# Optimization experiments

Hardware: AMD Instinct MI355X
Metric: run time of the kernel (lower is better)

The kernel has to match this reference:

```python
import jax, jax.numpy as jnp
import numpy as np

WS = 8          # window size
NUM_HEADS = 8


def setup_inputs() -> dict:
    key = jax.random.key(0)
    k1, k2, k3 = jax.random.split(key, 3)
    B, H, W, C = 8, 192, 192, 256
    x = jax.random.normal(k1, (B, H, W, C), dtype=jnp.float32)
    w_qkv = jax.random.normal(k2, (3 * C, C), dtype=jnp.float32) * (C ** -0.5)
    b_qkv = jnp.zeros((3 * C,), dtype=jnp.float32)
    w_proj = jax.random.normal(k3, (C, C), dtype=jnp.float32) * (C ** -0.5)
    b_proj = jnp.zeros((C,), dtype=jnp.float32)
    return {"x": x, "w_qkv": w_qkv, "b_qkv": b_qkv, "w_proj": w_proj, "b_proj": b_proj}


def _mhsa(tokens, w_qkv, b_qkv, w_proj, b_proj):
    # tokens: [Bgrp, N, C]
    Bg, N, C = tokens.shape
    d = C // NUM_HEADS
    qkv = tokens @ w_qkv.T + b_qkv                      # [Bg, N, 3C]
    qkv = qkv.reshape(Bg, N, 3, NUM_HEADS, d)
    q, k, v = [jnp.transpose(qkv[:, :, i], (0, 2, 1, 3)) for i in range(3)]  # [Bg, h, N, d]
    attn = jax.nn.softmax(jnp.einsum('bhnd,bhmd->bhnm', q, k) * (d ** -0.5), axis=-1)
    out = jnp.einsum('bhnm,bhmd->bhnd', attn, v)        # [Bg, h, N, d]
    out = jnp.transpose(out, (0, 2, 1, 3)).reshape(Bg, N, C)
    return out @ w_proj.T + b_proj


def reference(x, w_qkv, b_qkv, w_proj, b_proj):
    B, H, W, C = x.shape
    nH, nW = H // WS, W // WS
    # window partition: [B, H, W, C] -> [B*nH*nW, WS, WS, C]
    g = x.reshape(B, nH, WS, nW, WS, C).transpose(0, 1, 3, 2, 4, 5)
    tokens = g.reshape(B * nH * nW, WS * WS, C)
    tokens = _mhsa(tokens, w_qkv, b_qkv, w_proj, b_proj)
    # window unpartition
    g = tokens.reshape(B, nH, nW, WS, WS, C).transpose(0, 1, 3, 2, 4, 5)
    return g.reshape(B, H, W, C)
```

## Files before the change

### kernel.cpp

```cpp
#include <hip/hip_runtime.h>

typedef _Float16 half8  __attribute__((ext_vector_type(8)));
typedef _Float16 half4_t __attribute__((ext_vector_type(4)));
typedef __fp16   fp16x2 __attribute__((ext_vector_type(2)));
typedef float    f32x4  __attribute__((ext_vector_type(4)));

union PKU  { fp16x2 h; int i; };
union PK2  { fp16x2 h[2]; int i[2]; half4_t h4; };

__device__ __forceinline__ half4_t mk4(int a, int b) {
  PK2 u; u.i[0] = a; u.i[1] = b; return u.h4;
}

__device__ __forceinline__ int tokIdx(int r, int c) { return r*256 + (c ^ ((r & 7) << 3)); }

__global__ void __launch_bounds__(256)
wconv_kernel(const float* __restrict__ wq, const float* __restrict__ wp,
             _Float16* __restrict__ o)
{
  const int i = blockIdx.x * 256 + threadIdx.x;
  if (i < 768*256) o[i] = (_Float16)wq[i];
  else             o[i] = (_Float16)wp[i - 768*256];
}

__global__ void __launch_bounds__(256, 2)
attn_kernel(const float* __restrict__ x,
            const float* __restrict__ b_qkv,
            const float* __restrict__ b_proj,
            const _Float16* __restrict__ w16,
            float* __restrict__ out)
{
  __shared__ __align__(16) _Float16 tok[64*256];

  const int tid  = threadIdx.x;
  const int lane = tid & 63;
  const int w    = tid >> 6;
  const int l15  = lane & 15;
  const int g    = lane >> 4;

  const int wid = blockIdx.x;
  const int b   = wid / (24*24);
  const int wh  = (wid / 24) % 24;
  const int ww  = wid % 24;
  const long long base = (((long long)b*192 + wh*8)*192 + ww*8)*256;

#pragma unroll
  for (int i = 0; i < 16; ++i) {
    const int tk = w*16 + i;
    const float4 v = *(const float4*)(x + base + ((tk >> 3)*192 + (tk & 7))*256 + lane*4);
    half4_t h;
    h[0] = (_Float16)v.x; h[1] = (_Float16)v.y;
    h[2] = (_Float16)v.z; h[3] = (_Float16)v.w;
    *(half4_t*)(tok + tk*256 + ((lane*4) ^ ((tk & 7) << 3))) = h;
  }
  __syncthreads();

  const _Float16* wqkv16  = w16;
  const _Float16* wproj16 = w16 + 768*256;

  int ohp[2][2][4][2];

#pragma unroll
  for (int hi = 0; hi < 2; ++hi) {
    const int hd = 2*w + hi;

    f32x4 qa[2][4], kc[2][4], vv[4][2];
#pragma unroll
    for (int mi = 0; mi < 2; ++mi)
#pragma unroll
      for (int ni = 0; ni < 4; ++ni) { qa[mi][ni] = (f32x4)0.0f; kc[mi][ni] = (f32x4)0.0f; }
#pragma unroll
    for (int mi = 0; mi < 4; ++mi)
#pragma unroll
      for (int ni = 0; ni < 2; ++ni) vv[mi][ni] = (f32x4)0.0f;

#pragma unroll
    for (int kk = 0; kk < 8; ++kk) {
      half8 bt[4], aw[4], wv[2];
#pragma unroll
      for (int ni = 0; ni < 4; ++ni)
        bt[ni] = *(const half8*)(tok + tokIdx(ni*16 + l15, kk*32 + g*8));
#pragma unroll
      for (int mi = 0; mi < 2; ++mi) {
        aw[mi]     = *(const half8*)(wqkv16 + (      hd*32 + mi*16 + l15)*256 + kk*32 + g*8);
        aw[2 + mi] = *(const half8*)(wqkv16 + (256 + hd*32 + mi*16 + l15)*256 + kk*32 + g*8);
        wv[mi]     = *(const half8*)(wqkv16 + (512 + hd*32 + mi*16 + l15)*256 + kk*32 + g*8);
      }
      __builtin_amdgcn_s_setprio(1);
#pragma unroll
      for (int mi = 0; mi < 2; ++mi)
#pragma unroll
        for (int ni = 0; ni < 4; ++ni) {
          qa[mi][ni] = __builtin_amdgcn_mfma_f32_16x16x32_f16(aw[mi],     bt[ni], qa[mi][ni], 0, 0, 0);
          kc[mi][ni] = __builtin_amdgcn_mfma_f32_16x16x32_f16(aw[2 + mi], bt[ni], kc[mi][ni], 0, 0, 0);
        }
#pragma unroll
      for (int mi = 0; mi < 4; ++mi)
#pragma unroll
        for (int ni = 0; ni < 2; ++ni)
          vv[mi][ni] = __builtin_amdgcn_mfma_f32_16x16x32_f16(bt[mi], wv[ni], vv[mi][ni], 0, 0, 0);
      __builtin_amdgcn_s_setprio(0);
    }

    int qtp[2][4][2];
#pragma unroll
    for (int mi = 0; mi < 2; ++mi) {
      float bq[4];
#pragma unroll
      for (int r = 0; r < 4; ++r) bq[r] = b_qkv[hd*32 + mi*16 + g*4 + r];
#pragma unroll
      for (int ni = 0; ni < 4; ++ni) {
        PKU u0, u1;
        u0.h = __builtin_amdgcn_cvt_pkrtz(qa[mi][ni][0] + bq[0], qa[mi][ni][1] + bq[1]);
        u1.h = __builtin_amdgcn_cvt_pkrtz(qa[mi][ni][2] + bq[2], qa[mi][ni][3] + bq[3]);
        qtp[mi][ni][0] = u0.i; qtp[mi][ni][1] = u1.i;
      }
    }

    int kcp[2][4][2];
#pragma unroll
    for (int mi = 0; mi < 2; ++mi) {
      float bk[4];
#pragma unroll
      for (int r = 0; r < 4; ++r) bk[r] = b_qkv[256 + hd*32 + mi*16 + g*4 + r];
#pragma unroll
      for (int ni = 0; ni < 4; ++ni) {
        PKU u0, u1;
        u0.h = __builtin_amdgcn_cvt_pkrtz(kc[mi][ni][0] + bk[0], kc[mi][ni][1] + bk[1]);
        u1.h = __builtin_amdgcn_cvt_pkrtz(kc[mi][ni][2] + bk[2], kc[mi][ni][3] + bk[3]);
        kcp[mi][ni][0] = u0.i; kcp[mi][ni][1] = u1.i;
      }
    }

    int vpk[4][2][2];
#pragma unroll
    for (int ni = 0; ni < 2; ++ni) {
      const float bv = b_qkv[512 + hd*32 + ni*16 + l15];
#pragma unroll
      for (int mi = 0; mi < 4; ++mi) {
        PKU u0, u1;
        u0.h = __builtin_amdgcn_cvt_pkrtz(vv[mi][ni][0] + bv, vv[mi][ni][1] + bv);
        u1.h = __builtin_amdgcn_cvt_pkrtz(vv[mi][ni][2] + bv, vv[mi][ni][3] + bv);
        vpk[mi][ni][0] = u0.i;
        vpk[mi][ni][1] = u1.i;
      }
    }

    int pk[4][4][2];
    float rv[4];
    {
      f32x4 s[4][4];
#pragma unroll
      for (int MI = 0; MI < 4; ++MI)
#pragma unroll
        for (int ni = 0; ni < 4; ++ni) s[MI][ni] = (f32x4)0.0f;
      __builtin_amdgcn_s_setprio(1);
#pragma unroll
      for (int kk2 = 0; kk2 < 2; ++kk2)
#pragma unroll
        for (int ni = 0; ni < 4; ++ni) {
          const half4_t qb = mk4(qtp[kk2][ni][0], qtp[kk2][ni][1]);
#pragma unroll
          for (int MI = 0; MI < 4; ++MI)
            s[MI][ni] = __builtin_amdgcn_mfma_f32_16x16x16f16(
                mk4(kcp[kk2][MI][0], kcp[kk2][MI][1]), qb, s[MI][ni], 0, 0, 0);
        }
      __builtin_amdgcn_s_setprio(0);

      const float alpha = 0.17677669529663687f;
#pragma unroll
      for (int ni = 0; ni < 4; ++ni) {
        float m = s[0][ni][0];
#pragma unroll
        for (int MI = 0; MI < 4; ++MI)
#pragma unroll
          for (int r = 0; r < 4; ++r) m = fmaxf(m, s[MI][ni][r]);
        m = fmaxf(m, __shfl_xor(m, 16, 64));
        m = fmaxf(m, __shfl_xor(m, 32, 64));
        float sum = 0.0f;
#pragma unroll
        for (int MI = 0; MI < 4; ++MI)
#pragma unroll
          for (int r = 0; r < 4; ++r) {
            const float e = __expf((s[MI][ni][r] - m) * alpha);
            sum += e;
            s[MI][ni][r] = e;
          }
        sum += __shfl_xor(sum, 16, 64);
        sum += __shfl_xor(sum, 32, 64);
        rv[ni] = 1.0f / sum;
#pragma unroll
        for (int MI = 0; MI < 4; ++MI) {
          PKU u0, u1;
          u0.h = __builtin_amdgcn_cvt_pkrtz(s[MI][ni][0], s[MI][ni][1]);
          u1.h = __builtin_amdgcn_cvt_pkrtz(s[MI][ni][2], s[MI][ni][3]);
          pk[MI][ni][0] = u0.i;
          pk[MI][ni][1] = u1.i;
        }
      }
    }

    {
      f32x4 oh[2][4];
#pragma unroll
      for (int MI = 0; MI < 2; ++MI)
#pragma unroll
        for (int ni = 0; ni < 4; ++ni) oh[MI][ni] = (f32x4)0.0f;
      __builtin_amdgcn_s_setprio(1);
#pragma unroll
      for (int kk2 = 0; kk2 < 4; ++kk2)
#pragma unroll
        for (int ni = 0; ni < 4; ++ni) {
          const half4_t pb = mk4(pk[kk2][ni][0], pk[kk2][ni][1]);
#pragma unroll
          for (int MI = 0; MI < 2; ++MI)
            oh[MI][ni] = __builtin_amdgcn_mfma_f32_16x16x16f16(
                mk4(vpk[kk2][MI][0], vpk[kk2][MI][1]), pb, oh[MI][ni], 0, 0, 0);
        }
      __builtin_amdgcn_s_setprio(0);
#pragma unroll
      for (int MI = 0; MI < 2; ++MI)
#pragma unroll
        for (int ni = 0; ni < 4; ++ni) {
          PK2 u;
          u.h[0] = __builtin_amdgcn_cvt_pkrtz(oh[MI][ni][0] * rv[ni], oh[MI][ni][1] * rv[ni]);
          u.h[1] = __builtin_amdgcn_cvt_pkrtz(oh[MI][ni][2] * rv[ni], oh[MI][ni][3] * rv[ni]);
          ohp[hi][MI][ni][0] = u.i[0];
          ohp[hi][MI][ni][1] = u.i[1];
        }
    }
  }

  __syncthreads();

#pragma unroll
  for (int hi = 0; hi < 2; ++hi) {
    const int hd = 2*w + hi;
#pragma unroll
    for (int MI = 0; MI < 2; ++MI)
#pragma unroll
      for (int ni = 0; ni < 4; ++ni) {
        PK2 u;
        u.i[0] = ohp[hi][MI][ni][0];
        u.i[1] = ohp[hi][MI][ni][1];
        *(half4_t*)(tok + tokIdx(ni*16 + l15, hd*32 + MI*16 + g*4)) = u.h4;
      }
  }
  __syncthreads();

  f32x4 pa[4][4];
#pragma unroll
  for (int mi = 0; mi < 4; ++mi)
#pragma unroll
    for (int ni = 0; ni < 4; ++ni) pa[mi][ni] = (f32x4)0.0f;

#pragma unroll
  for (int kk = 0; kk < 8; ++kk) {
    half8 af[4], bf[4];
#pragma unroll
    for (int mi = 0; mi < 4; ++mi)
      af[mi] = *(const half8*)(tok + tokIdx(mi*16 + l15, kk*32 + g*8));
#pragma unroll
    for (int ni = 0; ni < 4; ++ni)
      bf[ni] = *(const half8*)(wproj16 + (w*64 + ni*16 + l15)*256 + kk*32 + g*8);
    __builtin_amdgcn_s_setprio(1);
#pragma unroll
    for (int mi = 0; mi < 4; ++mi)
#pragma unroll
      for (int ni = 0; ni < 4; ++ni)
        pa[mi][ni] = __builtin_amdgcn_mfma_f32_16x16x32_f16(af[mi], bf[ni], pa[mi][ni], 0, 0, 0);
    __builtin_amdgcn_s_setprio(0);
  }

#pragma unroll
  for (int ni = 0; ni < 4; ++ni) {
    const float bb = b_proj[w*64 + ni*16 + l15];
#pragma unroll
    for (int mi = 0; mi < 4; ++mi)
#pragma unroll
      for (int r = 0; r < 4; ++r) pa[mi][ni][r] += bb;
  }

  float* tokF = (float*)tok;
#pragma unroll
  for (int p = 0; p < 2; ++p) {
    __syncthreads();
#pragma unroll
    for (int mh = 0; mh < 2; ++mh) {
      const int mi = 2*p + mh;
#pragma unroll
      for (int ni = 0; ni < 4; ++ni)
#pragma unroll
        for (int r = 0; r < 4; ++r) {
          const int tr = mh*16 + g*4 + r;
          tokF[tr*256 + ((w*64 + ni*16 + l15) ^ ((tr & 7) << 2))] = pa[mi][ni][r];
        }
    }
    __syncthreads();
#pragma unroll
    for (int i = 0; i < 8; ++i) {
      const int tr = w*8 + i;
      const int t  = p*32 + tr;
      const long long rowbase = base + ((long long)(t >> 3)*192 + (t & 7))*256;
      const f32x4 v4 = *(const f32x4*)(tokF + tr*256 + ((lane*4) ^ ((tr & 7) << 2)));
      *(f32x4*)(out + rowbase + lane*4) = v4;
    }
  }
}

extern "C" void kernel_launch(void* const* d_in, const int* in_sizes, int n_in,
                              void* d_out, int out_size, void* d_ws, size_t ws_size,
                              hipStream_t stream) {
  const float* x      = (const float*)d_in[0];
  const float* w_qkv  = (const float*)d_in[1];
  const float* b_qkv  = (const float*)d_in[2];
  const float* w_proj = (const float*)d_in[3];
  const float* b_proj = (const float*)d_in[4];
  float* out = (float*)d_out;
  _Float16* w16 = (_Float16*)d_ws;

  wconv_kernel<<<1024, 256, 0, stream>>>(w_qkv, w_proj, w16);
  attn_kernel<<<4608, 256, 0, stream>>>(x, b_qkv, b_proj, w16, out);
}
```

Measured before the change: 356.5 us.

## Process two windows per block and prefetch the second window's input during compute

Each block now handles two adjacent windows, using a double-buffered LDS tile. The second window's x loads are issued in stages, interleaved with the first window's attention compute, and converted into the second buffer before it is needed, so global-load latency is hidden behind MFMA work. The weight conversion kernel is also vectorised to write 8 halves per thread. In exchange, LDS per block doubles to 64KB, which may limit occupancy at two blocks per CU, the extra prefetch registers add register pressure, and the grid is halved.

```diff
diff --git a/kernel.cpp b/kernel.cpp
--- a/kernel.cpp
+++ b/kernel.cpp
@@ -18,10 +18,22 @@
 wconv_kernel(const float* __restrict__ wq, const float* __restrict__ wp,
              _Float16* __restrict__ o)
 {
-  const int i = blockIdx.x * 256 + threadIdx.x;
-  if (i < 768*256) o[i] = (_Float16)wq[i];
-  else             o[i] = (_Float16)wp[i - 768*256];
+  const int i = (blockIdx.x * 256 + threadIdx.x) * 8;
+  const float4 a = *(const float4*)((i < 768*256 ? wq + i : wp + (i - 768*256)));
+  const float4 b = *(const float4*)((i < 768*256 ? wq + i + 4 : wp + (i - 768*256) + 4));
+  half8 h;
+  h[0] = (_Float16)a.x; h[1] = (_Float16)a.y; h[2] = (_Float16)a.z; h[3] = (_Float16)a.w;
+  h[4] = (_Float16)b.x; h[5] = (_Float16)b.y; h[6] = (_Float16)b.z; h[7] = (_Float16)b.w;
+  *(half8*)(o + i) = h;
 }
+
+#define LDX(s, j) (*(const f32x4*)(x + base1 + (((w*16 + (s)*4 + (j)) >> 3)*192 + ((w*16 + (s)*4 + (j)) & 7))*256 + lane*4))
+#define PF_ISSUE(s) { pf[0] = LDX(s,0); pf[1] = LDX(s,1); pf[2] = LDX(s,2); pf[3] = LDX(s,3); }
+#define STH(s, j) { const int tk = w*16 + (s)*4 + (j); half4_t h; \
+  h[0] = (_Float16)pf[j][0]; h[1] = (_Float16)pf[j][1]; \
+  h[2] = (_Float16)pf[j][2]; h[3] = (_Float16)pf[j][3]; \
+  *(half4_t*)(tok1 + tk*256 + ((lane*4) ^ ((tk & 7) << 3))) = h; }
+#define PF_COMMIT(s) { STH(s,0) STH(s,1) STH(s,2) STH(s,3) }
 
 __global__ void __launch_bounds__(256, 2)
 attn_kernel(const float* __restrict__ x,
@@ -30,7 +42,7 @@
             const _Float16* __restrict__ w16,
             float* __restrict__ out)
 {
-  __shared__ __align__(16) _Float16 tok[64*256];
+  __shared__ __align__(16) _Float16 tokbuf[2][64*256];
 
   const int tid  = threadIdx.x;
   const int lane = tid & 63;
@@ -38,273 +50,295 @@
   const int l15  = lane & 15;
   const int g    = lane >> 4;
 
-  const int wid = blockIdx.x;
-  const int b   = wid / (24*24);
-  const int wh  = (wid / 24) % 24;
-  const int ww  = wid % 24;
-  const long long base = (((long long)b*192 + wh*8)*192 + ww*8)*256;
+  const int W0  = blockIdx.x * 2;
+  const int b   = W0 / (24*24);
+  const int wh  = (W0 / 24) % 24;
+  const int ww  = W0 % 24;
+  const long long base0 = (((long long)b*192 + wh*8)*192 + ww*8)*256;
+  const long long base1 = base0 + 2048;
+
+  const _Float16* wqkv16  = w16;
+  const _Float16* wproj16 = w16 + 768*256;
+  _Float16* tok1 = &tokbuf[1][0];
+
+  f32x4 pf[4];
 
 #pragma unroll
   for (int i = 0; i < 16; ++i) {
     const int tk = w*16 + i;
-    const float4 v = *(const float4*)(x + base + ((tk >> 3)*192 + (tk & 7))*256 + lane*4);
+    const f32x4 v = *(const f32x4*)(x + base0 + ((tk >> 3)*192 + (tk & 7))*256 + lane*4);
     half4_t h;
-    h[0] = (_Float16)v.x; h[1] = (_Float16)v.y;
-    h[2] = (_Float16)v.z; h[3] = (_Float16)v.w;
-    *(half4_t*)(tok + tk*256 + ((lane*4) ^ ((tk & 7) << 3))) = h;
+    h[0] = (_Float16)v[0]; h[1] = (_Float16)v[1];
+    h[2] = (_Float16)v[2]; h[3] = (_Float16)v[3];
+    *(half4_t*)(tokbuf[0] + tk*256 + ((lane*4) ^ ((tk & 7) << 3))) = h;
   }
   __syncthreads();
 
-  const _Float16* wqkv16  = w16;
-  const _Float16* wproj16 = w16 + 768*256;
-
-  int ohp[2][2][4][2];
-
-#pragma unroll
-  for (int hi = 0; hi < 2; ++hi) {
-    const int hd = 2*w + hi;
-
-    f32x4 qa[2][4], kc[2][4], vv[4][2];
-#pragma unroll
-    for (int mi = 0; mi < 2; ++mi)
-#pragma unroll
-      for (int ni = 0; ni < 4; ++ni) { qa[mi][ni] = (f32x4)0.0f; kc[mi][ni] = (f32x4)0.0f; }
-#pragma unroll
-    for (int mi = 0; mi < 4; ++mi)
-#pragma unroll
-      for (int ni = 0; ni < 2; ++ni) vv[mi][ni] = (f32x4)0.0f;
-
-#pragma unroll
-    for (int kk = 0; kk < 8; ++kk) {
-      half8 bt[4], aw[4], wv[2];
-#pragma unroll
-      for (int ni = 0; ni < 4; ++ni)
-        bt[ni] = *(const half8*)(tok + tokIdx(ni*16 + l15, kk*32 + g*8));
+#pragma unroll
+  for (int wi = 0; wi < 2; ++wi) {
+    _Float16* tokc = &tokbuf[wi][0];
+    const long long basec = (wi == 0) ? base0 : base1;
+
+    int ohp[2][2][4][2];
+
+#pragma unroll
+    for (int hi = 0; hi < 2; ++hi) {
+      const int hd = 2*w + hi;
+
+      f32x4 qa[2][4], kc[2][4], vv[4][2];
+#pragma unroll
+      for (int mi = 0; mi < 2; ++mi)
+#pragma unroll
+        for (int ni = 0; ni < 4; ++ni) { qa[mi][ni] = (f32x4)0.0f; kc[mi][ni] = (f32x4)0.0f; }
+#pragma unroll
+      for (int mi = 0; mi < 4; ++mi)
+#pragma unroll
+        for (int ni = 0; ni < 2; ++ni) vv[mi][ni] = (f32x4)0.0f;
+
+#pragma unroll
+      for (int kk = 0; kk < 8; ++kk) {
+        half8 bt[4], aw[4], wvr[2];
+#pragma unroll
+        for (int ni = 0; ni < 4; ++ni)
+          bt[ni] = *(const half8*)(tokc + tokIdx(ni*16 + l15, kk*32 + g*8));
+#pragma unroll
+        for (int mi = 0; mi < 2; ++mi) {
+          aw[mi]     = *(const half8*)(wqkv16 + (      hd*32 + mi*16 + l15)*256 + kk*32 + g*8);
+          aw[2 + mi] = *(const half8*)(wqkv16 + (256 + hd*32 + mi*16 + l15)*256 + kk*32 + g*8);
+          wvr[mi]    = *(const half8*)(wqkv16 + (512 + hd*32 + mi*16 + l15)*256 + kk*32 + g*8);
+        }
+        __builtin_amdgcn_s_setprio(1);
+#pragma unroll
+        for (int mi = 0; mi < 2; ++mi)
+#pragma unroll
+          for (int ni = 0; ni < 4; ++ni) {
+            qa[mi][ni] = __builtin_amdgcn_mfma_f32_16x16x32_f16(aw[mi],     bt[ni], qa[mi][ni], 0, 0, 0);
+            kc[mi][ni] = __builtin_amdgcn_mfma_f32_16x16x32_f16(aw[2 + mi], bt[ni], kc[mi][ni], 0, 0, 0);
+          }
+#pragma unroll
+        for (int mi = 0; mi < 4; ++mi)
+#pragma unroll
+          for (int ni = 0; ni < 2; ++ni)
+            vv[mi][ni] = __builtin_amdgcn_mfma_f32_16x16x32_f16(bt[mi], wvr[ni], vv[mi][ni], 0, 0, 0);
+        __builtin_amdgcn_s_setprio(0);
+      }
+
+      if (wi == 0) {
+        if (hi == 0) { PF_ISSUE(0) }
+        else         { PF_COMMIT(1) PF_ISSUE(2) }
+      }
+
+      int qtp[2][4][2];
 #pragma unroll
       for (int mi = 0; mi < 2; ++mi) {
-        aw[mi]     = *(const half8*)(wqkv16 + (      hd*32 + mi*16 + l15)*256 + kk*32 + g*8);
-        aw[2 + mi] = *(const half8*)(wqkv16 + (256 + hd*32 + mi*16 + l15)*256 + kk*32 + g*8);
-        wv[mi]     = *(const half8*)(wqkv16 + (512 + hd*32 + mi*16 + l15)*256 + kk*32 + g*8);
-      }
-      __builtin_amdgcn_s_setprio(1);
-#pragma unroll
-      for (int mi = 0; mi < 2; ++mi)
+        float bq[4];
+#pragma unroll
+        for (int r = 0; r < 4; ++r) bq[r] = b_qkv[hd*32 + mi*16 + g*4 + r];
 #pragma unroll
         for (int ni = 0; ni < 4; ++ni) {
-          qa[mi][ni] = __builtin_amdgcn_mfma_f32_16x16x32_f16(aw[mi],     bt[ni], qa[mi][ni], 0, 0, 0);
-          kc[mi][ni] = __builtin_amdgcn_mfma_f32_16x16x32_f16(aw[2 + mi], bt[ni], kc[mi][ni], 0, 0, 0);
-        }
-#pragma unroll
-      for (int mi = 0; mi < 4; ++mi)
-#pragma unroll
-        for (int ni = 0; ni < 2; ++ni)
-          vv[mi][ni] = __builtin_amdgcn_mfma_f32_16x16x32_f16(bt[mi], wv[ni], vv[mi][ni], 0, 0, 0);
-      __builtin_amdgcn_s_setprio(0);
-    }
-
-    int qtp[2][4][2];
-#pragma unroll
-    for (int mi = 0; mi < 2; ++mi) {
-      float bq[4];
-#pragma unroll
-      for (int r = 0; r < 4; ++r) bq[r] = b_qkv[hd*32 + mi*16 + g*4 + r];
-#pragma unroll
-      for (int ni = 0; ni < 4; ++ni) {
-        PKU u0, u1;
-        u0.h = __builtin_amdgcn_cvt_pkrtz(qa[mi][ni][0] + bq[0], qa[mi][ni][1] + bq[1]);
-        u1.h = __builtin_amdgcn_cvt_pkrtz(qa[mi][ni][2] + bq[2], qa[mi][ni][3] + bq[3]);
-        qtp[mi][ni][0] = u0.i; qtp[mi][ni][1] = u1.i;
-      }
-    }
-
-    int kcp[2][4][2];
-#pragma unroll
-    for (int mi = 0; mi < 2; ++mi) {
-      float bk[4];
-#pragma unroll
-      for (int r = 0; r < 4; ++r) bk[r] = b_qkv[256 + hd*32 + mi*16 + g*4 + r];
-#pragma unroll
-      for (int ni = 0; ni < 4; ++ni) {
-        PKU u0, u1;
-        u0.h = __builtin_amdgcn_cvt_pkrtz(kc[mi][ni][0] + bk[0], kc[mi][ni][1] + bk[1]);
-        u1.h = __builtin_amdgcn_cvt_pkrtz(kc[mi][ni][2] + bk[2], kc[mi][ni][3] + bk[3]);
-        kcp[mi][ni][0] = u0.i; kcp[mi][ni][1] = u1.i;
-      }
-    }
-
-    int vpk[4][2][2];
-#pragma unroll
-    for (int ni = 0; ni < 2; ++ni) {
-      const float bv = b_qkv[512 + hd*32 + ni*16 + l15];
-#pragma unroll
-      for (int mi = 0; mi < 4; ++mi) {
-        PKU u0, u1;
-        u0.h = __builtin_amdgcn_cvt_pkrtz(vv[mi][ni][0] + bv, vv[mi][ni][1] + bv);
-        u1.h = __builtin_amdgcn_cvt_pkrtz(vv[mi][ni][2] + bv, vv[mi][ni][3] + bv);
-        vpk[mi][ni][0] = u0.i;
-        vpk[mi][ni][1] = u1.i;
-      }
-    }
-
-    int pk[4][4][2];
-    float rv[4];
-    {
-      f32x4 s[4][4];
-#pragma unroll
-      for (int MI = 0; MI < 4; ++MI)
-#pragma unroll
-        for (int ni = 0; ni < 4; ++ni) s[MI][ni] = (f32x4)0.0f;
-      __builtin_amdgcn_s_setprio(1);
-#pragma unroll
-      for (int kk2 = 0; kk2 < 2; ++kk2)
+          PKU u0, u1;
+          u0.h = __builtin_amdgcn_cvt_pkrtz(qa[mi][ni][0] + bq[0], qa[mi][ni][1] + bq[1]);
+          u1.h = __builtin_amdgcn_cvt_pkrtz(qa[mi][ni][2] + bq[2], qa[mi][ni][3] + bq[3]);
+          qtp[mi][ni][0] = u0.i; qtp[mi][ni][1] = u1.i;
+        }
+      }
+
+      int kcp[2][4][2];
+#pragma unroll
+      for (int mi = 0; mi < 2; ++mi) {
+        float bk[4];
+#pragma unroll
+        for (int r = 0; r < 4; ++r) bk[r] = b_qkv[256 + hd*32 + mi*16 + g*4 + r];
 #pragma unroll
         for (int ni = 0; ni < 4; ++ni) {
-          const half4_t qb = mk4(qtp[kk2][ni][0], qtp[kk2][ni][1]);
+          PKU u0, u1;
+          u0.h = __builtin_amdgcn_cvt_pkrtz(kc[mi][ni][0] + bk[0], kc[mi][ni][1] + bk[1]);
+          u1.h = __builtin_amdgcn_cvt_pkrtz(kc[mi][ni][2] + bk[2], kc[mi][ni][3] + bk[3]);
+          kcp[mi][ni][0] = u0.i; kcp[mi][ni][1] = u1.i;
+        }
+      }
+
+      int vpk[4][2][2];
+#pragma unroll
+      for (int ni = 0; ni < 2; ++ni) {
+        const float bv = b_qkv[512 + hd*32 + ni*16 + l15];
+#pragma unroll
+        for (int mi = 0; mi < 4; ++mi) {
+          PKU u0, u1;
+          u0.h = __builtin_amdgcn_cvt_pkrtz(vv[mi][ni][0] + bv, vv[mi][ni][1] + bv);
+          u1.h = __builtin_amdgcn_cvt_pkrtz(vv[mi][ni][2] + bv, vv[mi][ni][3] + bv);
+          vpk[mi][ni][0] = u0.i;
+          vpk[mi][ni][1] = u1.i;
+        }
+      }
+
+      int pk[4][4][2];
+      float rv[4];
+      {
+        f32x4 s[4][4];
+#pragma unroll
+        for (int MI = 0; MI < 4; ++MI)
+#pragma unroll
+          for (int ni = 0; ni < 4; ++ni) s[MI][ni] = (f32x4)0.0f;
+        __builtin_amdgcn_s_setprio(1);
+#pragma unroll
+        for (int kk2 = 0; kk2 < 2; ++kk2)
+#pragma unroll
+          for (int ni = 0; ni < 4; ++ni) {
+            const half4_t qb = mk4(qtp[kk2][ni][0], qtp[kk2][ni][1]);
+#pragma unroll
+            for (int MI = 0; MI < 4; ++MI)
+              s[MI][ni] = __builtin_amdgcn_mfma_f32_16x16x16f16(
+                  mk4(kcp[kk2][MI][0], kcp[kk2][MI][1]), qb, s[MI][ni], 0, 0, 0);
+          }
+        __builtin_amdgcn_s_setprio(0);
+
+        const float alpha = 0.17677669529663687f;
+#pragma unroll
+        for (int ni = 0; ni < 4; ++ni) {
+          float m = s[0][ni][0];
 #pragma unroll
           for (int MI = 0; MI < 4; ++MI)
-            s[MI][ni] = __builtin_amdgcn_mfma_f32_16x16x16f16(
-                mk4(kcp[kk2][MI][0], kcp[kk2][MI][1]), qb, s[MI][ni], 0, 0, 0);
-        }
-      __builtin_amdgcn_s_setprio(0);
-
-      const float alpha = 0.17677669529663687f;
-#pragma unroll
-      for (int ni = 0; ni < 4; ++ni) {
-        float m = s[0][ni][0];
-#pragma unroll
-        for (int MI = 0; MI < 4; ++MI)
-#pragma unroll
-          for (int r = 0; r < 4; ++r) m = fmaxf(m, s[MI][ni][r]);
-        m = fmaxf(m, __shfl_xor(m, 16, 64));
-        m = fmaxf(m, __shfl_xor(m, 32, 64));
-        float sum = 0.0f;
-#pragma unroll
-        for (int MI = 0; MI < 4; ++MI)
-#pragma unroll
-          for (int r = 0; r < 4; ++r) {
-            const float e = __expf((s[MI][ni][r] - m) * alpha);
-            sum += e;
-            s[MI][ni][r] = e;
-          }
-        sum += __shfl_xor(sum, 16, 64);
-        sum += __shfl_xor(sum, 32, 64);
-        rv[ni] = 1.0f / sum;
-#pragma unroll
-        for (int MI = 0; MI < 4; ++MI) {
-          PKU u0, u1;
-          u0.h = __builtin_amdgcn_cvt_pkrtz(s[MI][ni][0], s[MI][ni][1]);
-          u1.h = __builtin_amdgcn_cvt_pkrtz(s[MI][ni][2], s[MI][ni][3]);
-          pk[MI][ni][0] = u0.i;
-          pk[MI][ni][1] = u1.i;
-        }
-      }
-    }
-
-    {
-      f32x4 oh[2][4];
-#pragma unroll
-      for (int MI = 0; MI < 2; ++MI)
-#pragma unroll
-        for (int ni = 0; ni < 4; ++ni) oh[MI][ni] = (f32x4)0.0f;
-      __builtin_amdgcn_s_setprio(1);
-#pragma unroll
-      for (int kk2 = 0; kk2 < 4; ++kk2)
-#pragma unroll
-        for (int ni = 0; ni < 4; ++ni) {
-          const half4_t pb = mk4(pk[kk2][ni][0], pk[kk2][ni][1]);
-#pragma unroll
-          for (int MI = 0; MI < 2; ++MI)
-            oh[MI][ni] = __builtin_amdgcn_mfma_f32_16x16x16f16(
-                mk4(vpk[kk2][MI][0], vpk[kk2][MI][1]), pb, oh[MI][ni], 0, 0, 0);
-        }
-      __builtin_amdgcn_s_setprio(0);
+#pragma unroll
+            for (int r = 0; r < 4; ++r) m = fmaxf(m, s[MI][ni][r]);
+          m = fmaxf(m, __shfl_xor(m, 16, 64));
+          m = fmaxf(m, __shfl_xor(m, 32, 64));
+          float sum = 0.0f;
+#pragma unroll
+          for (int MI = 0; MI < 4; ++MI)
+#pragma unroll
+            for (int r = 0; r < 4; ++r) {
+              const float e = __expf((s[MI][ni][r] - m) * alpha);
+              sum += e;
+              s[MI][ni][r] = e;
+            }
+          sum += __shfl_xor(sum, 16, 64);
+          sum += __shfl_xor(sum, 32, 64);
+          rv[ni] = 1.0f / sum;
+#pragma unroll
+          for (int MI = 0; MI < 4; ++MI) {
+            PKU u0, u1;
+            u0.h = __builtin_amdgcn_cvt_pkrtz(s[MI][ni][0], s[MI][ni][1]);
+            u1.h = __builtin_amdgcn_cvt_pkrtz(s[MI][ni][2], s[MI][ni][3]);
+            pk[MI][ni][0] = u0.i;
+            pk[MI][ni][1] = u1.i;
+          }
+        }
+      }
+
+      {
+        f32x4 oh[2][4];
+#pragma unroll
+        for (int MI = 0; MI < 2; ++MI)
+#pragma unroll
+          for (int ni = 0; ni < 4; ++ni) oh[MI][ni] = (f32x4)0.0f;
+        __builtin_amdgcn_s_setprio(1);
+#pragma unroll
+        for (int kk2 = 0; kk2 < 4; ++kk2)
+#pragma unroll
+          for (int ni = 0; ni < 4; ++ni) {
+            const half4_t pb = mk4(pk[kk2][ni][0], pk[kk2][ni][1]);
+#pragma unroll
+            for (int MI = 0; MI < 2; ++MI)
+              oh[MI][ni] = __builtin_amdgcn_mfma_f32_16x16x16f16(
+                  mk4(vpk[kk2][MI][0], vpk[kk2][MI][1]), pb, oh[MI][ni], 0, 0, 0);
+          }
+        __builtin_amdgcn_s_setprio(0);
+#pragma unroll
+        for (int MI = 0; MI < 2; ++MI)
+#pragma unroll
+          for (int ni = 0; ni < 4; ++ni) {
+            PK2 u;
+            u.h[0] = __builtin_amdgcn_cvt_pkrtz(oh[MI][ni][0] * rv[ni], oh[MI][ni][1] * rv[ni]);
+            u.h[1] = __builtin_amdgcn_cvt_pkrtz(oh[MI][ni][2] * rv[ni], oh[MI][ni][3] * rv[ni]);
+            ohp[hi][MI][ni][0] = u.i[0];
+            ohp[hi][MI][ni][1] = u.i[1];
+          }
+      }
+
+      if (wi == 0) {
+        if (hi == 0) { PF_COMMIT(0) PF_ISSUE(1) }
+        else         { PF_COMMIT(2) PF_ISSUE(3) }
+      }
+    }
+
+    __syncthreads();
+
+#pragma unroll
+    for (int hi = 0; hi < 2; ++hi) {
+      const int hd = 2*w + hi;
 #pragma unroll
       for (int MI = 0; MI < 2; ++MI)
 #pragma unroll
         for (int ni = 0; ni < 4; ++ni) {
           PK2 u;
-          u.h[0] = __builtin_amdgcn_cvt_pkrtz(oh[MI][ni][0] * rv[ni], oh[MI][ni][1] * rv[ni]);
-          u.h[1] = __builtin_amdgcn_cvt_pkrtz(oh[MI][ni][2] * rv[ni], oh[MI][ni][3] * rv[ni]);
-          ohp[hi][MI][ni][0] = u.i[0];
-          ohp[hi][MI][ni][1] = u.i[1];
-        }
-    }
-  }
-
-  __syncthreads();
-
-#pragma unroll
-  for (int hi = 0; hi < 2; ++hi) {
-    const int hd = 2*w + hi;
-#pragma unroll
-    for (int MI = 0; MI < 2; ++MI)
-#pragma unroll
-      for (int ni = 0; ni < 4; ++ni) {
-        PK2 u;
-        u.i[0] = ohp[hi][MI][ni][0];
-        u.i[1] = ohp[hi][MI][ni][1];
-        *(half4_t*)(tok + tokIdx(ni*16 + l15, hd*32 + MI*16 + g*4)) = u.h4;
-      }
-  }
-  __syncthreads();
-
-  f32x4 pa[4][4];
-#pragma unroll
-  for (int mi = 0; mi < 4; ++mi)
-#pragma unroll
-    for (int ni = 0; ni < 4; ++ni) pa[mi][ni] = (f32x4)0.0f;
-
-#pragma unroll
-  for (int kk = 0; kk < 8; ++kk) {
-    half8 af[4], bf[4];
+          u.i[0] = ohp[hi][MI][ni][0];
+          u.i[1] = ohp[hi][MI][ni][1];
+          *(half4_t*)(tokc + tokIdx(ni*16 + l15, hd*32 + MI*16 + g*4)) = u.h4;
+        }
+    }
+    if (wi == 0) { PF_COMMIT(3) }
+    __syncthreads();
+
+    f32x4 pa[4][4];
 #pragma unroll
     for (int mi = 0; mi < 4; ++mi)
-      af[mi] = *(const half8*)(tok + tokIdx(mi*16 + l15, kk*32 + g*8));
-#pragma unroll
-    for (int ni = 0; ni < 4; ++ni)
-      bf[ni] = *(const half8*)(wproj16 + (w*64 + ni*16 + l15)*256 + kk*32 + g*8);
-    __builtin_amdgcn_s_setprio(1);
-#pragma unroll
-    for (int mi = 0; mi < 4; ++mi)
+#pragma unroll
+      for (int ni = 0; ni < 4; ++ni) pa[mi][ni] = (f32x4)0.0f;
+
+#pragma unroll
+    for (int kk = 0; kk < 8; ++kk) {
+      half8 af[4], bf[4];
+#pragma unroll
+      for (int mi = 0; mi < 4; ++mi)
+        af[mi] = *(const half8*)(tokc + tokIdx(mi*16 + l15, kk*32 + g*8));
 #pragma unroll
       for (int ni = 0; ni < 4; ++ni)
-        pa[mi][ni] = __builtin_amdgcn_mfma_f32_16x16x32_f16(af[mi], bf[ni], pa[mi][ni], 0, 0, 0);
-    __builtin_amdgcn_s_setprio(0);
-  }
-
-#pragma unroll
-  for (int ni = 0; ni < 4; ++ni) {
-    const float bb = b_proj[w*64 + ni*16 + l15];
-#pragma unroll
-    for (int mi = 0; mi < 4; ++mi)
-#pragma unroll
-      for (int r = 0; r < 4; ++r) pa[mi][ni][r] += bb;
-  }
-
-  float* tokF = (float*)tok;
-#pragma unroll
-  for (int p = 0; p < 2; ++p) {
-    __syncthreads();
-#pragma unroll
-    for (int mh = 0; mh < 2; ++mh) {
-      const int mi = 2*p + mh;
-#pragma unroll
-      for (int ni = 0; ni < 4; ++ni)
-#pragma unroll
-        for (int r = 0; r < 4; ++r) {
-          const int tr = mh*16 + g*4 + r;
-          tokF[tr*256 + ((w*64 + ni*16 + l15) ^ ((tr & 7) << 2))] = pa[mi][ni][r];
-        }
-    }
-    __syncthreads();
-#pragma unroll
-    for (int i = 0; i < 8; ++i) {
-      const int tr = w*8 + i;
-      const int t  = p*32 + tr;
-      const long long rowbase = base + ((long long)(t >> 3)*192 + (t & 7))*256;
-      const f32x4 v4 = *(const f32x4*)(tokF + tr*256 + ((lane*4) ^ ((tr & 7) << 2)));
-      *(f32x4*)(out + rowbase + lane*4) = v4;
-    }
+        bf[ni] = *(const half8*)(wproj16 + (w*64 + ni*16 + l15)*256 + kk*32 + g*8);
+      __builtin_amdgcn_s_setprio(1);
+#pragma unroll
+      for (int mi = 0; mi < 4; ++mi)
+#pragma unroll
+        for (int ni = 0; ni < 4; ++ni)
+          pa[mi][ni] = __builtin_amdgcn_mfma_f32_16x16x32_f16(af[mi], bf[ni], pa[mi][ni], 0, 0, 0);
+      __builtin_amdgcn_s_setprio(0);
+    }
+
+#pragma unroll
+    for (int ni = 0; ni < 4; ++ni) {
+      const float bb = b_proj[w*64 + ni*16 + l15];
+#pragma unroll
+      for (int mi = 0; mi < 4; ++mi)
+#pragma unroll
+        for (int r = 0; r < 4; ++r) pa[mi][ni][r] += bb;
+    }
+
+    float* tokF = (float*)tokc;
+#pragma unroll
+    for (int p = 0; p < 2; ++p) {
+      __syncthreads();
+#pragma unroll
+      for (int mh = 0; mh < 2; ++mh) {
+        const int mi = 2*p + mh;
+#pragma unroll
+        for (int ni = 0; ni < 4; ++ni)
+#pragma unroll
+          for (int r = 0; r < 4; ++r) {
+            const int tr = mh*16 + g*4 + r;
+            tokF[tr*256 + ((w*64 + ni*16 + l15) ^ ((tr & 7) << 2))] = pa[mi][ni][r];
+          }
+      }
+      __syncthreads();
+#pragma unroll
+      for (int i = 0; i < 8; ++i) {
+        const int tr = w*8 + i;
+        const int t  = p*32 + tr;
+        const long long rowbase = basec + ((long long)(t >> 3)*192 + (t & 7))*256;
+        const f32x4 v4 = *(const f32x4*)(tokF + tr*256 + ((lane*4) ^ ((tr & 7) << 2)));
+        *(f32x4*)(out + rowbase + lane*4) = v4;
+      }
+    }
+    if (wi == 0) __syncthreads();
   }
 }
 
@@ -319,6 +353,6 @@
   float* out = (float*)d_out;
   _Float16* w16 = (_Float16*)d_ws;
 
-  wconv_kernel<<<1024, 256, 0, stream>>>(w_qkv, w_proj, w16);
-  attn_kernel<<<4608, 256, 0, stream>>>(x, b_qkv, b_proj, w16, out);
+  wconv_kernel<<<128, 256, 0, stream>>>(w_qkv, w_proj, w16);
+  attn_kernel<<<2304, 256, 0, stream>>>(x, b_qkv, b_proj, w16, out);
 }
```

New measurement: 476.8 us. 33.8% more time.

## Split QKV projection into phases to cut registers and raise occupancy

Applied to the files above, without the earlier changes.

Computes Q, K and V projections in three separate loops instead of one fused loop, and splits the score/softmax stage into two halves, so fewer accumulators are live at once. The launch bound goes from 2 to 4 blocks per SM to use the freed registers. The softmax scale is folded into Q before the fp16 conversion, and the weight conversion kernel is vectorized to 8 elements per thread. In exchange, the token tile is re-read from shared memory three times, and spills are possible if the register budget is exceeded.

```diff
diff --git a/kernel.cpp b/kernel.cpp
--- a/kernel.cpp
+++ b/kernel.cpp
@@ -18,12 +18,16 @@
 wconv_kernel(const float* __restrict__ wq, const float* __restrict__ wp,
              _Float16* __restrict__ o)
 {
-  const int i = blockIdx.x * 256 + threadIdx.x;
-  if (i < 768*256) o[i] = (_Float16)wq[i];
-  else             o[i] = (_Float16)wp[i - 768*256];
+  const int i = (blockIdx.x * 256 + threadIdx.x) * 8;
+  const float4 a = *(const float4*)((i < 768*256 ? wq + i : wp + (i - 768*256)));
+  const float4 b = *(const float4*)((i < 768*256 ? wq + i + 4 : wp + (i - 768*256) + 4));
+  half8 h;
+  h[0] = (_Float16)a.x; h[1] = (_Float16)a.y; h[2] = (_Float16)a.z; h[3] = (_Float16)a.w;
+  h[4] = (_Float16)b.x; h[5] = (_Float16)b.y; h[6] = (_Float16)b.z; h[7] = (_Float16)b.w;
+  *(half8*)(o + i) = h;
 }
 
-__global__ void __launch_bounds__(256, 2)
+__global__ void __launch_bounds__(256, 4)
 attn_kernel(const float* __restrict__ x,
             const float* __restrict__ b_qkv,
             const float* __restrict__ b_proj,
@@ -47,10 +51,10 @@
 #pragma unroll
   for (int i = 0; i < 16; ++i) {
     const int tk = w*16 + i;
-    const float4 v = *(const float4*)(x + base + ((tk >> 3)*192 + (tk & 7))*256 + lane*4);
+    const f32x4 v = *(const f32x4*)(x + base + ((tk >> 3)*192 + (tk & 7))*256 + lane*4);
     half4_t h;
-    h[0] = (_Float16)v.x; h[1] = (_Float16)v.y;
-    h[2] = (_Float16)v.z; h[3] = (_Float16)v.w;
+    h[0] = (_Float16)v[0]; h[1] = (_Float16)v[1];
+    h[2] = (_Float16)v[2]; h[3] = (_Float16)v[3];
     *(half4_t*)(tok + tk*256 + ((lane*4) ^ ((tk & 7) << 3))) = h;
   }
   __syncthreads();
@@ -58,123 +62,161 @@
   const _Float16* wqkv16  = w16;
   const _Float16* wproj16 = w16 + 768*256;
 
+  const float ALPHA = 0.17677669529663687f;
+
   int ohp[2][2][4][2];
 
 #pragma unroll
   for (int hi = 0; hi < 2; ++hi) {
     const int hd = 2*w + hi;
 
-    f32x4 qa[2][4], kc[2][4], vv[4][2];
-#pragma unroll
-    for (int mi = 0; mi < 2; ++mi)
-#pragma unroll
-      for (int ni = 0; ni < 4; ++ni) { qa[mi][ni] = (f32x4)0.0f; kc[mi][ni] = (f32x4)0.0f; }
-#pragma unroll
-    for (int mi = 0; mi < 4; ++mi)
-#pragma unroll
-      for (int ni = 0; ni < 2; ++ni) vv[mi][ni] = (f32x4)0.0f;
-
-#pragma unroll
-    for (int kk = 0; kk < 8; ++kk) {
-      half8 bt[4], aw[4], wv[2];
-#pragma unroll
-      for (int ni = 0; ni < 4; ++ni)
-        bt[ni] = *(const half8*)(tok + tokIdx(ni*16 + l15, kk*32 + g*8));
+    int qtp[2][4][2];
+    {
+      f32x4 qa[2][4];
+#pragma unroll
+      for (int mi = 0; mi < 2; ++mi)
+#pragma unroll
+        for (int ni = 0; ni < 4; ++ni) qa[mi][ni] = (f32x4)0.0f;
+#pragma unroll
+      for (int kk = 0; kk < 8; ++kk) {
+        half8 bt[4], aw[2];
+#pragma unroll
+        for (int ni = 0; ni < 4; ++ni)
+          bt[ni] = *(const half8*)(tok + tokIdx(ni*16 + l15, kk*32 + g*8));
+#pragma unroll
+        for (int mi = 0; mi < 2; ++mi)
+          aw[mi] = *(const half8*)(wqkv16 + (hd*32 + mi*16 + l15)*256 + kk*32 + g*8);
+        __builtin_amdgcn_s_setprio(1);
+#pragma unroll
+        for (int mi = 0; mi < 2; ++mi)
+#pragma unroll
+          for (int ni = 0; ni < 4; ++ni)
+            qa[mi][ni] = __builtin_amdgcn_mfma_f32_16x16x32_f16(aw[mi], bt[ni], qa[mi][ni], 0, 0, 0);
+        __builtin_amdgcn_s_setprio(0);
+      }
 #pragma unroll
       for (int mi = 0; mi < 2; ++mi) {
-        aw[mi]     = *(const half8*)(wqkv16 + (      hd*32 + mi*16 + l15)*256 + kk*32 + g*8);
-        aw[2 + mi] = *(const half8*)(wqkv16 + (256 + hd*32 + mi*16 + l15)*256 + kk*32 + g*8);
-        wv[mi]     = *(const half8*)(wqkv16 + (512 + hd*32 + mi*16 + l15)*256 + kk*32 + g*8);
-      }
-      __builtin_amdgcn_s_setprio(1);
+        float bq[4];
+#pragma unroll
+        for (int r = 0; r < 4; ++r) bq[r] = b_qkv[hd*32 + mi*16 + g*4 + r];
+#pragma unroll
+        for (int ni = 0; ni < 4; ++ni) {
+          PKU u0, u1;
+          u0.h = __builtin_amdgcn_cvt_pkrtz((qa[mi][ni][0] + bq[0])*ALPHA, (qa[mi][ni][1] + bq[1])*ALPHA);
+          u1.h = __builtin_amdgcn_cvt_pkrtz((qa[mi][ni][2] + bq[2])*ALPHA, (qa[mi][ni][3] + bq[3])*ALPHA);
+          qtp[mi][ni][0] = u0.i; qtp[mi][ni][1] = u1.i;
+        }
+      }
+    }
+
+    int kcp[2][4][2];
+    {
+      f32x4 kc[2][4];
 #pragma unroll
       for (int mi = 0; mi < 2; ++mi)
 #pragma unroll
+        for (int ni = 0; ni < 4; ++ni) kc[mi][ni] = (f32x4)0.0f;
+#pragma unroll
+      for (int kk = 0; kk < 8; ++kk) {
+        half8 bt[4], aw[2];
+#pragma unroll
+        for (int ni = 0; ni < 4; ++ni)
+          bt[ni] = *(const half8*)(tok + tokIdx(ni*16 + l15, kk*32 + g*8));
+#pragma unroll
+        for (int mi = 0; mi < 2; ++mi)
+          aw[mi] = *(const half8*)(wqkv16 + (256 + hd*32 + mi*16 + l15)*256 + kk*32 + g*8);
+        __builtin_amdgcn_s_setprio(1);
+#pragma unroll
+        for (int mi = 0; mi < 2; ++mi)
+#pragma unroll
+          for (int ni = 0; ni < 4; ++ni)
+            kc[mi][ni] = __builtin_amdgcn_mfma_f32_16x16x32_f16(aw[mi], bt[ni], kc[mi][ni], 0, 0, 0);
+        __builtin_amdgcn_s_setprio(0);
+      }
+#pragma unroll
+      for (int mi = 0; mi < 2; ++mi) {
+        float bk[4];
+#pragma unroll
+        for (int r = 0; r < 4; ++r) bk[r] = b_qkv[256 + hd*32 + mi*16 + g*4 + r];
+#pragma unroll
         for (int ni = 0; ni < 4; ++ni) {
-          qa[mi][ni] = __builtin_amdgcn_mfma_f32_16x16x32_f16(aw[mi],     bt[ni], qa[mi][ni], 0, 0, 0);
-          kc[mi][ni] = __builtin_amdgcn_mfma_f32_16x16x32_f16(aw[2 + mi], bt[ni], kc[mi][ni], 0, 0, 0);
-        }
+          PKU u0, u1;
+          u0.h = __builtin_amdgcn_cvt_pkrtz(kc[mi][ni][0] + bk[0], kc[mi][ni][1] + bk[1]);
+          u1.h = __builtin_amdgcn_cvt_pkrtz(kc[mi][ni][2] + bk[2], kc[mi][ni][3] + bk[3]);
+          kcp[mi][ni][0] = u0.i; kcp[mi][ni][1] = u1.i;
+        }
+      }
+    }
+
+    int vpk[4][2][2];
+    {
+      f32x4 vv[4][2];
 #pragma unroll
       for (int mi = 0; mi < 4; ++mi)
 #pragma unroll
+        for (int ni = 0; ni < 2; ++ni) vv[mi][ni] = (f32x4)0.0f;
+#pragma unroll
+      for (int kk = 0; kk < 8; ++kk) {
+        half8 bt[4], wv[2];
+#pragma unroll
+        for (int mi = 0; mi < 4; ++mi)
+          bt[mi] = *(const half8*)(tok + tokIdx(mi*16 + l15, kk*32 + g*8));
+#pragma unroll
         for (int ni = 0; ni < 2; ++ni)
-          vv[mi][ni] = __builtin_amdgcn_mfma_f32_16x16x32_f16(bt[mi], wv[ni], vv[mi][ni], 0, 0, 0);
-      __builtin_amdgcn_s_setprio(0);
-    }
-
-    int qtp[2][4][2];
-#pragma unroll
-    for (int mi = 0; mi < 2; ++mi) {
-      float bq[4];
-#pragma unroll
-      for (int r = 0; r < 4; ++r) bq[r] = b_qkv[hd*32 + mi*16 + g*4 + r];
-#pragma unroll
-      for (int ni = 0; ni < 4; ++ni) {
-        PKU u0, u1;
-        u0.h = __builtin_amdgcn_cvt_pkrtz(qa[mi][ni][0] + bq[0], qa[mi][ni][1] + bq[1]);
-        u1.h = __builtin_amdgcn_cvt_pkrtz(qa[mi][ni][2] + bq[2], qa[mi][ni][3] + bq[3]);
-        qtp[mi][ni][0] = u0.i; qtp[mi][ni][1] = u1.i;
-      }
-    }
-
-    int kcp[2][4][2];
-#pragma unroll
-    for (int mi = 0; mi < 2; ++mi) {
-      float bk[4];
-#pragma unroll
-      for (int r = 0; r < 4; ++r) bk[r] = b_qkv[256 + hd*32 + mi*16 + g*4 + r];
-#pragma unroll
-      for (int ni = 0; ni < 4; ++ni) {
-        PKU u0, u1;
-        u0.h = __builtin_amdgcn_cvt_pkrtz(kc[mi][ni][0] + bk[0], kc[mi][ni][1] + bk[1]);
-        u1.h = __builtin_amdgcn_cvt_pkrtz(kc[mi][ni][2] + bk[2], kc[mi][ni][3] + bk[3]);
-        kcp[mi][ni][0] = u0.i; kcp[mi][ni][1] = u1.i;
-      }
-    }
-
-    int vpk[4][2][2];
-#pragma unroll
-    for (int ni = 0; ni < 2; ++ni) {
-      const float bv = b_qkv[512 + hd*32 + ni*16 + l15];
-#pragma unroll
-      for (int mi = 0; mi < 4; ++mi) {
-        PKU u0, u1;
-        u0.h = __builtin_amdgcn_cvt_pkrtz(vv[mi][ni][0] + bv, vv[mi][ni][1] + bv);
-        u1.h = __builtin_amdgcn_cvt_pkrtz(vv[mi][ni][2] + bv, vv[mi][ni][3] + bv);
-        vpk[mi][ni][0] = u0.i;
-        vpk[mi][ni][1] = u1.i;
+          wv[ni] = *(const half8*)(wqkv16 + (512 + hd*32 + ni*16 + l15)*256 + kk*32 + g*8);
+        __builtin_amdgcn_s_setprio(1);
+#pragma unroll
+        for (int mi = 0; mi < 4; ++mi)
+#pragma unroll
+          for (int ni = 0; ni < 2; ++ni)
+            vv[mi][ni] = __builtin_amdgcn_mfma_f32_16x16x32_f16(bt[mi], wv[ni], vv[mi][ni], 0, 0, 0);
+        __builtin_amdgcn_s_setprio(0);
+      }
+#pragma unroll
+      for (int ni = 0; ni < 2; ++ni) {
+        const float bv = b_qkv[512 + hd*32 + ni*16 + l15];
+#pragma unroll
+        for (int mi = 0; mi < 4; ++mi) {
+          PKU u0, u1;
+          u0.h = __builtin_amdgcn_cvt_pkrtz(vv[mi][ni][0] + bv, vv[mi][ni][1] + bv);
+          u1.h = __builtin_amdgcn_cvt_pkrtz(vv[mi][ni][2] + bv, vv[mi][ni][3] + bv);
+          vpk[mi][ni][0] = u0.i;
+          vpk[mi][ni][1] = u1.i;
+        }
       }
     }
 
     int pk[4][4][2];
     float rv[4];
-    {
-      f32x4 s[4][4];
+#pragma unroll
+    for (int pr = 0; pr < 2; ++pr) {
+      f32x4 s[4][2];
 #pragma unroll
       for (int MI = 0; MI < 4; ++MI)
 #pragma unroll
-        for (int ni = 0; ni < 4; ++ni) s[MI][ni] = (f32x4)0.0f;
+        for (int nj = 0; nj < 2; ++nj) s[MI][nj] = (f32x4)0.0f;
       __builtin_amdgcn_s_setprio(1);
 #pragma unroll
       for (int kk2 = 0; kk2 < 2; ++kk2)
 #pragma unroll
-        for (int ni = 0; ni < 4; ++ni) {
+        for (int nj = 0; nj < 2; ++nj) {
+          const int ni = pr*2 + nj;
           const half4_t qb = mk4(qtp[kk2][ni][0], qtp[kk2][ni][1]);
 #pragma unroll
           for (int MI = 0; MI < 4; ++MI)
-            s[MI][ni] = __builtin_amdgcn_mfma_f32_16x16x16f16(
-                mk4(kcp[kk2][MI][0], kcp[kk2][MI][1]), qb, s[MI][ni], 0, 0, 0);
+            s[MI][nj] = __builtin_amdgcn_mfma_f32_16x16x16f16(
+                mk4(kcp[kk2][MI][0], kcp[kk2][MI][1]), qb, s[MI][nj], 0, 0, 0);
         }
       __builtin_amdgcn_s_setprio(0);
 
-      const float alpha = 0.17677669529663687f;
-#pragma unroll
-      for (int ni = 0; ni < 4; ++ni) {
-        float m = s[0][ni][0];
+#pragma unroll
+      for (int nj = 0; nj < 2; ++nj) {
+        const int ni = pr*2 + nj;
+        float m = s[0][nj][0];
 #pragma unroll
         for (int MI = 0; MI < 4; ++MI)
 #pragma unroll
-          for (int r = 0; r < 4; ++r) m = fmaxf(m, s[MI][ni][r]);
+          for (int r = 0; r < 4; ++r) m = fmaxf(m, s[MI][nj][r]);
         m = fmaxf(m, __shfl_xor(m, 16, 64));
         m = fmaxf(m, __shfl_xor(m, 32, 64));
         float sum = 0.0f;
@@ -182,9 +224,9 @@
         for (int MI = 0; MI < 4; ++MI)
 #pragma unroll
           for (int r = 0; r < 4; ++r) {
-            const float e = __expf((s[MI][ni][r] - m) * alpha);
+            const float e = __expf(s[MI][nj][r] - m);
             sum += e;
-            s[MI][ni][r] = e;
+            s[MI][nj][r] = e;
           }
         sum += __shfl_xor(sum, 16, 64);
         sum += __shfl_xor(sum, 32, 64);
@@ -192,8 +234,8 @@
 #pragma unroll
         for (int MI = 0; MI < 4; ++MI) {
           PKU u0, u1;
-          u0.h = __builtin_amdgcn_cvt_pkrtz(s[MI][ni][0], s[MI][ni][1]);
-          u1.h = __builtin_amdgcn_cvt_pkrtz(s[MI][ni][2], s[MI][ni][3]);
+          u0.h = __builtin_amdgcn_cvt_pkrtz(s[MI][nj][0], s[MI][nj][1]);
+          u1.h = __builtin_amdgcn_cvt_pkrtz(s[MI][nj][2], s[MI][nj][3]);
           pk[MI][ni][0] = u0.i;
           pk[MI][ni][1] = u1.i;
         }
@@ -319,6 +361,6 @@
   float* out = (float*)d_out;
   _Float16* w16 = (_Float16*)d_ws;
 
-  wconv_kernel<<<1024, 256, 0, stream>>>(w_qkv, w_proj, w16);
+  wconv_kernel<<<128, 256, 0, stream>>>(w_qkv, w_proj, w16);
   attn_kernel<<<4608, 256, 0, stream>>>(x, b_qkv, b_proj, w16, out);
 }
```

After: 383.9 us. 7.7% more time.
